# Kernel optimization log

Hardware: AMD Instinct MI355X
Metric: run time of the kernel (lower is better)

Reference implementation:

```python
import jax, jax.numpy as jnp
import numpy as np

B, L, D, H = 2, 2048, 768, 12
HD = D // H  # 64
BASE = 10000


def rope_tables(seq_len, head_dim, base):
    # inverse frequencies over even indices, angles [L, hd/2] -> duplicated to [L, hd]
    inv_freq = 1.0 / (base ** (jnp.arange(0, head_dim, 2, dtype=jnp.float32) / head_dim))
    angles = jnp.arange(seq_len, dtype=jnp.float32)[:, None] * inv_freq[None, :]
    cos = jnp.concatenate([jnp.cos(angles), jnp.cos(angles)], axis=-1)  # [L, hd]
    sin = jnp.concatenate([jnp.sin(angles), jnp.sin(angles)], axis=-1)
    return cos, sin


def rotate_half(x):
    x1, x2 = jnp.split(x, 2, axis=-1)
    return jnp.concatenate([-x2, x1], axis=-1)


def setup_inputs() -> dict:
    key = jax.random.key(0)
    k0, k1, k2 = jax.random.split(key, 3)
    s = 0.02
    return {
        "input_embeddings": jax.random.normal(k0, (B, L, D), dtype=jnp.float32),
        "w_qkv": jax.random.normal(k1, (D, 3 * D), dtype=jnp.float32) * s,
        "b_qkv": jnp.zeros((3 * D,), dtype=jnp.float32),
        "w_out": jax.random.normal(k2, (D, D), dtype=jnp.float32) * s,
        "b_out": jnp.zeros((D,), dtype=jnp.float32),
    }


def reference(input_embeddings, w_qkv, b_qkv, w_out, b_out):
    # QKV projection and head split: b l (h d) -> b h l d
    qkv = input_embeddings @ w_qkv + b_qkv
    q, k, v = jnp.split(qkv, 3, axis=-1)
    to_heads = lambda t: t.reshape(B, L, H, HD).transpose(0, 2, 1, 3)
    q, k, v = map(to_heads, (q, k, v))

    # RoPE (start_pos=0, no kv cache)
    cos, sin = rope_tables(L, HD, BASE)  # [L, HD], broadcasts over b,h
    q = q * cos + rotate_half(q) * sin
    k = k * cos + rotate_half(k) * sin

    # NOTE: source divides by sqrt(d.size(3)) = sqrt(key_seq_len), not sqrt(head_dim)
    scores = jnp.einsum("bhqd,bhkd->bhqk", q, k) / jnp.sqrt(jnp.float32(L))

    causal_mask = jnp.triu(jnp.ones((L, L), dtype=bool), 1)
    neg_inf = -jnp.finfo(scores.dtype).max
    scores = jnp.where(causal_mask, neg_inf, scores)

    probs = jax.nn.softmax(scores, axis=-1)  # dropout disabled (eval)
    attn_out = jnp.einsum("bhqk,bhkd->bhqd", probs, v)
    attn_out = attn_out.transpose(0, 2, 1, 3).reshape(B, L, D)  # b h l d -> b l (h d)
    output = attn_out @ w_out + b_out
    return output, probs
```

## Files before the change

kernel.cpp:

```cpp
#include <hip/hip_runtime.h>
#include <math.h>

#define B_  2
#define L_  2048
#define D_  768
#define H_  12
#define HD_ 64
#define M_  (B_*L_)
#define N3_ (3*D_)
#define OUT_ELEMS ((size_t)B_*L_*D_)

static constexpr float kScale = 0.022097086912079608f;
static constexpr float kLog2_10000_div32 = 0.415241011860920f;

typedef __attribute__((ext_vector_type(8))) short short8;
typedef __attribute__((ext_vector_type(4))) float f32x4;

__device__ __forceinline__ unsigned short f2bf(float f) {
  union { float f; unsigned u; } v; v.f = f;
  unsigned r = v.u + 0x7FFFu + ((v.u >> 16) & 1u);
  return (unsigned short)(r >> 16);
}

__device__ __forceinline__ void async_cp16(const void* g, void* l) {
  __builtin_amdgcn_global_load_lds((const __attribute__((address_space(1))) void*)g,
                                   (__attribute__((address_space(3))) void*)l, 16, 0, 0);
}

__global__ __launch_bounds__(256) void bf16conv_kernel(const float* __restrict__ in,
                                                       unsigned short* __restrict__ out)
{
  const int idx = blockIdx.x * 256 + threadIdx.x;
  const float* src = in + (size_t)idx * 8;
  float4 a = *(const float4*)src;
  float4 b = *(const float4*)(src + 4);
  unsigned short t[8];
  t[0] = f2bf(a.x); t[1] = f2bf(a.y); t[2] = f2bf(a.z); t[3] = f2bf(a.w);
  t[4] = f2bf(b.x); t[5] = f2bf(b.y); t[6] = f2bf(b.z); t[7] = f2bf(b.w);
  *(uint4*)(out + (size_t)idx * 8) = *(uint4*)t;
}

__global__ __launch_bounds__(256) void wtrans_kernel(const float* __restrict__ in,
                                                     unsigned short* __restrict__ out,
                                                     int K, int N)
{
  __shared__ __align__(16) unsigned short T[64][72];
  const int n0 = blockIdx.x * 64;
  const int k0 = blockIdx.y * 64;
  const int tid = threadIdx.x;
  const int row = tid >> 2;
  const int col = (tid & 3) * 16;
  {
    const float* src = in + (size_t)(k0 + row) * N + n0 + col;
    unsigned short tmp[16];
#pragma unroll
    for (int j = 0; j < 16; j += 4) {
      float4 v = *(const float4*)(src + j);
      tmp[j] = f2bf(v.x); tmp[j + 1] = f2bf(v.y); tmp[j + 2] = f2bf(v.z); tmp[j + 3] = f2bf(v.w);
    }
    *(uint4*)&T[row][col]     = *(uint4*)tmp;
    *(uint4*)&T[row][col + 8] = *(uint4*)(tmp + 8);
  }
  __syncthreads();
  unsigned short tmp[16];
#pragma unroll
  for (int j = 0; j < 16; ++j) tmp[j] = T[col + j][row];
  unsigned short* dst = out + (size_t)(n0 + row) * K + k0 + col;
  *(uint4*)dst       = *(uint4*)tmp;
  *(uint4*)(dst + 8) = *(uint4*)(tmp + 8);
}

__global__ __launch_bounds__(256) void vtrans_kernel(const unsigned short* __restrict__ vb,
                                                     unsigned short* __restrict__ vt)
{
  __shared__ __align__(16) unsigned short T[64][72];
  const int bh = blockIdx.y;
  const int l0 = blockIdx.x * 64;
  const int tid = threadIdx.x;
  const int row = tid >> 2;
  const int col = (tid & 3) * 16;
  {
    const unsigned short* src = vb + ((size_t)bh * L_ + l0 + row) * HD_ + col;
    *(uint4*)&T[row][col]     = *(const uint4*)src;
    *(uint4*)&T[row][col + 8] = *(const uint4*)(src + 8);
  }
  __syncthreads();
  unsigned short tmp[16];
#pragma unroll
  for (int j = 0; j < 16; ++j) tmp[j] = T[col + j][row];
  unsigned short* dst = vt + ((size_t)bh * HD_ + row) * L_ + l0 + col;
  *(uint4*)dst       = *(uint4*)tmp;
  *(uint4*)(dst + 8) = *(uint4*)(tmp + 8);
}

__global__ __launch_bounds__(256) void gemm_mfma_kernel(
    const unsigned short* __restrict__ A, const unsigned short* __restrict__ Bt,
    const float* __restrict__ bias, float* __restrict__ C,
    int M, int N, int K, int mode,
    unsigned short* __restrict__ qp, unsigned short* __restrict__ kp,
    unsigned short* __restrict__ vp)
{
  __shared__ __align__(16) unsigned short As[2][128 * 32];
  __shared__ __align__(16) unsigned short Bs[2][128 * 32];

  const int tid  = threadIdx.x;
  const int w    = tid >> 6;
  const int lane = tid & 63;
  const int m16  = lane & 15;
  const int quad = lane >> 4;
  const int wr   = w & 1;
  const int wc   = w >> 1;

  const int bm = blockIdx.y * 128;
  const int bn = blockIdx.x * 128;

  const int s0 = w * 128 + lane;
  const int s1 = s0 + 64;
  const int r0 = s0 >> 2, c0 = (s0 & 3) ^ (r0 & 3);
  const int r1 = s1 >> 2, c1 = (s1 & 3) ^ (r1 & 3);
  const unsigned short* gA0 = A + (size_t)(bm + r0) * K + c0 * 8;
  const unsigned short* gA1 = A + (size_t)(bm + r1) * K + c1 * 8;
  const unsigned short* gB0 = Bt + (size_t)(bn + r0) * K + c0 * 8;
  const unsigned short* gB1 = Bt + (size_t)(bn + r1) * K + c1 * 8;
  const int oS0 = (w * 128) * 8;
  const int oS1 = (w * 128 + 64) * 8;

  const int sw = quad ^ (m16 & 3);
  int offA[4], offB[4];
#pragma unroll
  for (int i = 0; i < 4; ++i) {
    const int ra = wr * 64 + i * 16 + m16;
    const int rb = wc * 64 + i * 16 + m16;
    offA[i] = ra * 32 + sw * 8;
    offB[i] = rb * 32 + sw * 8;
  }

  f32x4 acc[4][4];
#pragma unroll
  for (int i = 0; i < 4; ++i)
#pragma unroll
    for (int j = 0; j < 4; ++j) { acc[i][j][0] = 0.f; acc[i][j][1] = 0.f; acc[i][j][2] = 0.f; acc[i][j][3] = 0.f; }

  async_cp16(gA0, &As[0][oS0]);
  async_cp16(gA1, &As[0][oS1]);
  async_cp16(gB0, &Bs[0][oS0]);
  async_cp16(gB1, &Bs[0][oS1]);
  __syncthreads();

  int cur = 0;
  for (int k0 = 0; k0 < K; k0 += 32) {
    const int nk = k0 + 32;
    if (nk < K) {
      unsigned short* an = &As[cur ^ 1][0];
      unsigned short* bn2 = &Bs[cur ^ 1][0];
      async_cp16(gA0 + nk, an + oS0);
      async_cp16(gA1 + nk, an + oS1);
      async_cp16(gB0 + nk, bn2 + oS0);
      async_cp16(gB1 + nk, bn2 + oS1);
    }
    const unsigned short* Ac = &As[cur][0];
    const unsigned short* Bc = &Bs[cur][0];
    short8 af[4], bfr[4];
#pragma unroll
    for (int i = 0; i < 4; ++i) {
      af[i]  = *(const short8*)(Ac + offA[i]);
      bfr[i] = *(const short8*)(Bc + offB[i]);
    }
#pragma unroll
    for (int i = 0; i < 4; ++i)
#pragma unroll
      for (int j = 0; j < 4; ++j)
        acc[i][j] = __builtin_amdgcn_mfma_f32_16x16x32_bf16(af[i], bfr[j], acc[i][j], 0, 0, 0);
    __syncthreads();
    cur ^= 1;
  }

  if (mode == 0) {
#pragma unroll
    for (int j = 0; j < 4; ++j) {
      const int n = bn + wc * 64 + j * 16 + m16;
      const float bj = bias[n];
#pragma unroll
      for (int i = 0; i < 4; ++i) {
        const int mrow = bm + wr * 64 + i * 16 + quad * 4;
#pragma unroll
        for (int r2 = 0; r2 < 4; ++r2)
          C[(size_t)(mrow + r2) * N + n] = acc[i][j][r2] + bj;
      }
    }
  } else {
    const int segbase = bn + wc * 64;
    const int which = segbase / D_;
    const int h = (segbase - which * D_) >> 6;
    unsigned short* dstT = (which == 0) ? qp : (which == 1) ? kp : vp;
    float bj[4];
#pragma unroll
    for (int og = 0; og < 4; ++og) bj[og] = bias[segbase + og * 16 + m16];
    const float invfA = exp2f(-(float)m16 * kLog2_10000_div32);
    const float invfB = exp2f(-(float)(16 + m16) * kLog2_10000_div32);

#pragma unroll
    for (int i = 0; i < 4; ++i) {
      const int mrow = bm + wr * 64 + i * 16 + quad * 4;
#pragma unroll
      for (int r2 = 0; r2 < 4; ++r2) {
        const int m = mrow + r2;
        const int bi = m >> 11;
        const int li = m & (L_ - 1);
        float vals[4];
#pragma unroll
        for (int og = 0; og < 4; ++og) vals[og] = acc[i][og][r2] + bj[og];
        unsigned short* drow = dstT + (((size_t)(bi * H_ + h)) * L_ + li) * HD_;
        if (which == 2) {
#pragma unroll
          for (int og = 0; og < 4; ++og) drow[og * 16 + m16] = f2bf(vals[og]);
        } else {
          const float fl = (float)li;
#pragma unroll
          for (int og = 0; og < 4; ++og) {
            const int d = og * 16 + m16;
            const float theta = fl * ((og & 1) ? invfB : invfA);
            float sv, cv;
            __sincosf(theta, &sv, &cv);
            const float part = vals[og ^ 2];
            const float rot = (og < 2) ? -part : part;
            drow[d] = f2bf(vals[og] * cv + rot * sv);
          }
        }
      }
    }
  }
}

__global__ __launch_bounds__(256) void attn_mfma_kernel(
    const unsigned short* __restrict__ qb, const unsigned short* __restrict__ kb,
    const unsigned short* __restrict__ vt, float* __restrict__ probs,
    unsigned short* __restrict__ attnb)
{
  __shared__ __align__(16) unsigned short Vs[2][64 * 64];
  __shared__ __align__(16) unsigned short Pb[4][16][72];

  const int tid  = threadIdx.x;
  const int w    = tid >> 6;
  const int lane = tid & 63;
  const int m16  = lane & 15;
  const int quad = lane >> 4;

  const int bh = blockIdx.y;
  const int qt = (int)gridDim.x - 1 - (int)blockIdx.x;
  const int q0 = qt * 64;
  const int bb = bh / H_;
  const int hh = bh - bb * H_;
  const int ktiles = qt + 1;
  const int qrow_base = q0 + w * 16;

  const unsigned short* kbase = kb + (size_t)bh * L_ * HD_;
  const unsigned short* vbase = vt + (size_t)bh * HD_ * L_;

  const unsigned short* qp = qb + ((size_t)bh * L_ + qrow_base + m16) * HD_ + quad * 8;
  const short8 qf0 = *(const short8*)(qp);
  const short8 qf1 = *(const short8*)(qp + 32);

  const unsigned short* kfp = kbase + (size_t)m16 * HD_ + quad * 8;

  float lsum[4] = {0.f, 0.f, 0.f, 0.f};
  for (int kt = 0; kt < ktiles; ++kt) {
    const int k0 = kt * 64;
    short8 kb0[4], kb1[4];
#pragma unroll
    for (int cg = 0; cg < 4; ++cg) {
      const unsigned short* kr = kfp + (size_t)(k0 + cg * 16) * HD_;
      kb0[cg] = *(const short8*)(kr);
      kb1[cg] = *(const short8*)(kr + 32);
    }
#pragma unroll
    for (int cg = 0; cg < 4; ++cg) {
      f32x4 s = {0.f, 0.f, 0.f, 0.f};
      s = __builtin_amdgcn_mfma_f32_16x16x32_bf16(qf0, kb0[cg], s, 0, 0, 0);
      s = __builtin_amdgcn_mfma_f32_16x16x32_bf16(qf1, kb1[cg], s, 0, 0, 0);
      const int kcol = k0 + cg * 16 + m16;
#pragma unroll
      for (int r2 = 0; r2 < 4; ++r2) {
        const int qrow = qrow_base + quad * 4 + r2;
        const float e = __expf(s[r2] * kScale);
        lsum[r2] += (kcol <= qrow) ? e : 0.f;
      }
    }
  }
  float linv[4];
#pragma unroll
  for (int r2 = 0; r2 < 4; ++r2) {
    float v = lsum[r2];
    v += __shfl_xor(v, 1, 64);
    v += __shfl_xor(v, 2, 64);
    v += __shfl_xor(v, 4, 64);
    v += __shfl_xor(v, 8, 64);
    linv[r2] = 1.f / v;
  }

  f32x4 oacc[4];
#pragma unroll
  for (int og = 0; og < 4; ++og) { oacc[og][0]=0.f; oacc[og][1]=0.f; oacc[og][2]=0.f; oacc[og][3]=0.f; }

  const int vs0 = w * 64 + lane;
  const int vs1 = vs0 + 256;
  const int vr0 = vs0 >> 3, vc0 = ((vs0 & 7) ^ (vr0 & 7)) * 8;
  const int vr1 = vs1 >> 3, vc1 = ((vs1 & 7) ^ (vr1 & 7)) * 8;
  const unsigned short* gV0 = vbase + (size_t)vr0 * L_ + vc0;
  const unsigned short* gV1 = vbase + (size_t)vr1 * L_ + vc1;
  const int oV0 = (w * 64) * 8;
  const int oV1 = 2048 + (w * 64) * 8;
  const int swv = m16 & 7;

  async_cp16(gV0, &Vs[0][oV0]);
  async_cp16(gV1, &Vs[0][oV1]);
  __syncthreads();

  int cur = 0;
  for (int kt = 0; kt < ktiles; ++kt) {
    const int k0 = kt * 64;
    if (kt + 1 < ktiles) {
      unsigned short* nb = &Vs[cur ^ 1][0];
      async_cp16(gV0 + k0 + 64, nb + oV0);
      async_cp16(gV1 + k0 + 64, nb + oV1);
    }
    short8 kb0[4], kb1[4];
#pragma unroll
    for (int cg = 0; cg < 4; ++cg) {
      const unsigned short* kr = kfp + (size_t)(k0 + cg * 16) * HD_;
      kb0[cg] = *(const short8*)(kr);
      kb1[cg] = *(const short8*)(kr + 32);
    }
#pragma unroll
    for (int cg = 0; cg < 4; ++cg) {
      f32x4 s = {0.f, 0.f, 0.f, 0.f};
      s = __builtin_amdgcn_mfma_f32_16x16x32_bf16(qf0, kb0[cg], s, 0, 0, 0);
      s = __builtin_amdgcn_mfma_f32_16x16x32_bf16(qf1, kb1[cg], s, 0, 0, 0);
      const int kcol = k0 + cg * 16 + m16;
#pragma unroll
      for (int r2 = 0; r2 < 4; ++r2) {
        const int qrow = qrow_base + quad * 4 + r2;
        const float p = (kcol <= qrow) ? __expf(s[r2] * kScale) * linv[r2] : 0.f;
        probs[((size_t)bh * L_ + qrow) * L_ + kcol] = p;
        Pb[w][quad * 4 + r2][cg * 16 + m16] = f2bf(p);
      }
    }
    const short8 pa0 = *(const short8*)&Pb[w][m16][quad * 8];
    const short8 pa1 = *(const short8*)&Pb[w][m16][32 + quad * 8];
    const unsigned short* Vb = &Vs[cur][0];
#pragma unroll
    for (int og = 0; og < 4; ++og) {
      const int r = og * 16 + m16;
      const short8 v0 = *(const short8*)(Vb + r * 64 + ((quad ^ swv) * 8));
      const short8 v1 = *(const short8*)(Vb + r * 64 + (((quad + 4) ^ swv) * 8));
      oacc[og] = __builtin_amdgcn_mfma_f32_16x16x32_bf16(pa0, v0, oacc[og], 0, 0, 0);
      oacc[og] = __builtin_amdgcn_mfma_f32_16x16x32_bf16(pa1, v1, oacc[og], 0, 0, 0);
    }
    __syncthreads();
    cur ^= 1;
  }

#pragma unroll
  for (int og = 0; og < 4; ++og)
#pragma unroll
    for (int r2 = 0; r2 < 4; ++r2)
      attnb[((size_t)bb * L_ + qrow_base + quad * 4 + r2) * D_ + hh * HD_ + og * 16 + m16] =
          f2bf(oacc[og][r2]);

  {
    const f32x4 z4 = {0.f, 0.f, 0.f, 0.f};
#pragma unroll
    for (int r2 = 0; r2 < 4; ++r2) {
      float* pr = probs + ((size_t)bh * L_ + qrow_base + quad * 4 + r2) * L_;
      for (int c0z = ktiles * 64; c0z < L_; c0z += 64)
        *(f32x4*)(pr + c0z + m16 * 4) = z4;
    }
  }
}

extern "C" void kernel_launch(void* const* d_in, const int* in_sizes, int n_in,
                              void* d_out, int out_size, void* d_ws, size_t ws_size,
                              hipStream_t stream)
{
  const float* x     = (const float*)d_in[0];
  const float* w_qkv = (const float*)d_in[1];
  const float* b_qkv = (const float*)d_in[2];
  const float* w_out = (const float*)d_in[3];
  const float* b_out = (const float*)d_in[4];

  float* out   = (float*)d_out;
  float* probs = out + OUT_ELEMS;

  const size_t NE = (size_t)B_ * H_ * L_ * HD_;
  unsigned short* qbw   = (unsigned short*)d_ws;
  unsigned short* kbw   = qbw + NE;
  unsigned short* vbw   = kbw + NE;
  unsigned short* vtw   = vbw + NE;
  unsigned short* xbw   = vtw + NE;
  unsigned short* attnb = xbw + NE;
  unsigned short* wqT   = attnb + NE;
  unsigned short* woT   = wqT + (size_t)N3_ * D_;

  bf16conv_kernel<<<(int)(OUT_ELEMS / 8 / 256), 256, 0, stream>>>(x, xbw);
  wtrans_kernel<<<dim3(N3_ / 64, D_ / 64), 256, 0, stream>>>(w_qkv, wqT, D_, N3_);
  wtrans_kernel<<<dim3(D_ / 64, D_ / 64), 256, 0, stream>>>(w_out, woT, D_, D_);

  gemm_mfma_kernel<<<dim3(N3_ / 128, M_ / 128), 256, 0, stream>>>(
      xbw, wqT, b_qkv, nullptr, M_, N3_, D_, 1, qbw, kbw, vbw);

  vtrans_kernel<<<dim3(L_ / 64, B_ * H_), 256, 0, stream>>>(vbw, vtw);

  attn_mfma_kernel<<<dim3(L_ / 64, B_ * H_), 256, 0, stream>>>(qbw, kbw, vtw, probs, attnb);

  gemm_mfma_kernel<<<dim3(D_ / 128, M_ / 128), 256, 0, stream>>>(
      attnb, woT, b_out, out, M_, D_, D_, 0, nullptr, nullptr, nullptr);
}
```

Measured before the change: 620.9 us.

## Stage K tiles in shared memory with async double-buffering in both attention passes

K tiles are now loaded cooperatively into swizzled, double-buffered LDS with async copies in both the row-sum pass and the output pass. Previously each wave read K directly from global memory, so the four waves of a block fetched the same K data redundantly. The second pass also raises wave priority around the PV MFMA block. This adds 16 KB of LDS and an extra barrier per tile in the first pass, which may reduce occupancy.

```diff
diff --git a/kernel.cpp b/kernel.cpp
--- a/kernel.cpp
+++ b/kernel.cpp
@@ -237,6 +237,7 @@
     const unsigned short* __restrict__ vt, float* __restrict__ probs,
     unsigned short* __restrict__ attnb)
 {
+  __shared__ __align__(16) unsigned short Ks[2][64 * 64];
   __shared__ __align__(16) unsigned short Vs[2][64 * 64];
   __shared__ __align__(16) unsigned short Pb[4][16][72];
 
@@ -261,30 +262,49 @@
   const short8 qf0 = *(const short8*)(qp);
   const short8 qf1 = *(const short8*)(qp + 32);
 
-  const unsigned short* kfp = kbase + (size_t)m16 * HD_ + quad * 8;
+  const int s0g = tid, s1g = tid + 256;
+  const int r0 = s0g >> 3, c0 = (s0g & 7) ^ (r0 & 7);
+  const int r1 = s1g >> 3, c1 = (s1g & 7) ^ (r1 & 7);
+  const unsigned short* gK0 = kbase + (size_t)r0 * HD_ + c0 * 8;
+  const unsigned short* gK1 = kbase + (size_t)r1 * HD_ + c1 * 8;
+  const unsigned short* gV0 = vbase + (size_t)r0 * L_ + c0 * 8;
+  const unsigned short* gV1 = vbase + (size_t)r1 * L_ + c1 * 8;
+  const int oL0 = (w * 64) * 8;
+  const int oL1 = (256 + w * 64) * 8;
+  const int swk = m16 & 7;
 
   float lsum[4] = {0.f, 0.f, 0.f, 0.f};
-  for (int kt = 0; kt < ktiles; ++kt) {
-    const int k0 = kt * 64;
-    short8 kb0[4], kb1[4];
-#pragma unroll
-    for (int cg = 0; cg < 4; ++cg) {
-      const unsigned short* kr = kfp + (size_t)(k0 + cg * 16) * HD_;
-      kb0[cg] = *(const short8*)(kr);
-      kb1[cg] = *(const short8*)(kr + 32);
-    }
-#pragma unroll
-    for (int cg = 0; cg < 4; ++cg) {
-      f32x4 s = {0.f, 0.f, 0.f, 0.f};
-      s = __builtin_amdgcn_mfma_f32_16x16x32_bf16(qf0, kb0[cg], s, 0, 0, 0);
-      s = __builtin_amdgcn_mfma_f32_16x16x32_bf16(qf1, kb1[cg], s, 0, 0, 0);
-      const int kcol = k0 + cg * 16 + m16;
-#pragma unroll
-      for (int r2 = 0; r2 < 4; ++r2) {
-        const int qrow = qrow_base + quad * 4 + r2;
-        const float e = __expf(s[r2] * kScale);
-        lsum[r2] += (kcol <= qrow) ? e : 0.f;
-      }
+  {
+    async_cp16(gK0, &Ks[0][oL0]);
+    async_cp16(gK1, &Ks[0][oL1]);
+    __syncthreads();
+    int cur = 0;
+    for (int kt = 0; kt < ktiles; ++kt) {
+      const int k0 = kt * 64;
+      if (kt + 1 < ktiles) {
+        const size_t adv = (size_t)(kt + 1) * 64 * HD_;
+        async_cp16(gK0 + adv, &Ks[cur ^ 1][oL0]);
+        async_cp16(gK1 + adv, &Ks[cur ^ 1][oL1]);
+      }
+      const unsigned short* Kc = &Ks[cur][0];
+#pragma unroll
+      for (int cg = 0; cg < 4; ++cg) {
+        const int r = cg * 16 + m16;
+        const short8 b0 = *(const short8*)(Kc + r * 64 + ((quad ^ swk) * 8));
+        const short8 b1 = *(const short8*)(Kc + r * 64 + (((quad + 4) ^ swk) * 8));
+        f32x4 s = {0.f, 0.f, 0.f, 0.f};
+        s = __builtin_amdgcn_mfma_f32_16x16x32_bf16(qf0, b0, s, 0, 0, 0);
+        s = __builtin_amdgcn_mfma_f32_16x16x32_bf16(qf1, b1, s, 0, 0, 0);
+        const int kcol = k0 + cg * 16 + m16;
+#pragma unroll
+        for (int r2 = 0; r2 < 4; ++r2) {
+          const int qrow = qrow_base + quad * 4 + r2;
+          const float e = __expf(s[r2] * kScale);
+          lsum[r2] += (kcol <= qrow) ? e : 0.f;
+        }
+      }
+      __syncthreads();
+      cur ^= 1;
     }
   }
   float linv[4];
@@ -302,62 +322,57 @@
 #pragma unroll
   for (int og = 0; og < 4; ++og) { oacc[og][0]=0.f; oacc[og][1]=0.f; oacc[og][2]=0.f; oacc[og][3]=0.f; }
 
-  const int vs0 = w * 64 + lane;
-  const int vs1 = vs0 + 256;
-  const int vr0 = vs0 >> 3, vc0 = ((vs0 & 7) ^ (vr0 & 7)) * 8;
-  const int vr1 = vs1 >> 3, vc1 = ((vs1 & 7) ^ (vr1 & 7)) * 8;
-  const unsigned short* gV0 = vbase + (size_t)vr0 * L_ + vc0;
-  const unsigned short* gV1 = vbase + (size_t)vr1 * L_ + vc1;
-  const int oV0 = (w * 64) * 8;
-  const int oV1 = 2048 + (w * 64) * 8;
-  const int swv = m16 & 7;
-
-  async_cp16(gV0, &Vs[0][oV0]);
-  async_cp16(gV1, &Vs[0][oV1]);
-  __syncthreads();
-
-  int cur = 0;
-  for (int kt = 0; kt < ktiles; ++kt) {
-    const int k0 = kt * 64;
-    if (kt + 1 < ktiles) {
-      unsigned short* nb = &Vs[cur ^ 1][0];
-      async_cp16(gV0 + k0 + 64, nb + oV0);
-      async_cp16(gV1 + k0 + 64, nb + oV1);
-    }
-    short8 kb0[4], kb1[4];
-#pragma unroll
-    for (int cg = 0; cg < 4; ++cg) {
-      const unsigned short* kr = kfp + (size_t)(k0 + cg * 16) * HD_;
-      kb0[cg] = *(const short8*)(kr);
-      kb1[cg] = *(const short8*)(kr + 32);
-    }
-#pragma unroll
-    for (int cg = 0; cg < 4; ++cg) {
-      f32x4 s = {0.f, 0.f, 0.f, 0.f};
-      s = __builtin_amdgcn_mfma_f32_16x16x32_bf16(qf0, kb0[cg], s, 0, 0, 0);
-      s = __builtin_amdgcn_mfma_f32_16x16x32_bf16(qf1, kb1[cg], s, 0, 0, 0);
-      const int kcol = k0 + cg * 16 + m16;
-#pragma unroll
-      for (int r2 = 0; r2 < 4; ++r2) {
-        const int qrow = qrow_base + quad * 4 + r2;
-        const float p = (kcol <= qrow) ? __expf(s[r2] * kScale) * linv[r2] : 0.f;
-        probs[((size_t)bh * L_ + qrow) * L_ + kcol] = p;
-        Pb[w][quad * 4 + r2][cg * 16 + m16] = f2bf(p);
-      }
-    }
-    const short8 pa0 = *(const short8*)&Pb[w][m16][quad * 8];
-    const short8 pa1 = *(const short8*)&Pb[w][m16][32 + quad * 8];
-    const unsigned short* Vb = &Vs[cur][0];
-#pragma unroll
-    for (int og = 0; og < 4; ++og) {
-      const int r = og * 16 + m16;
-      const short8 v0 = *(const short8*)(Vb + r * 64 + ((quad ^ swv) * 8));
-      const short8 v1 = *(const short8*)(Vb + r * 64 + (((quad + 4) ^ swv) * 8));
-      oacc[og] = __builtin_amdgcn_mfma_f32_16x16x32_bf16(pa0, v0, oacc[og], 0, 0, 0);
-      oacc[og] = __builtin_amdgcn_mfma_f32_16x16x32_bf16(pa1, v1, oacc[og], 0, 0, 0);
-    }
+  {
+    async_cp16(gK0, &Ks[0][oL0]);
+    async_cp16(gK1, &Ks[0][oL1]);
+    async_cp16(gV0, &Vs[0][oL0]);
+    async_cp16(gV1, &Vs[0][oL1]);
     __syncthreads();
-    cur ^= 1;
+    int cur = 0;
+    for (int kt = 0; kt < ktiles; ++kt) {
+      const int k0 = kt * 64;
+      if (kt + 1 < ktiles) {
+        const size_t advK = (size_t)(kt + 1) * 64 * HD_;
+        const int advV = (kt + 1) * 64;
+        async_cp16(gK0 + advK, &Ks[cur ^ 1][oL0]);
+        async_cp16(gK1 + advK, &Ks[cur ^ 1][oL1]);
+        async_cp16(gV0 + advV, &Vs[cur ^ 1][oL0]);
+        async_cp16(gV1 + advV, &Vs[cur ^ 1][oL1]);
+      }
+      const unsigned short* Kc = &Ks[cur][0];
+      const unsigned short* Vc = &Vs[cur][0];
+#pragma unroll
+      for (int cg = 0; cg < 4; ++cg) {
+        const int r = cg * 16 + m16;
+        const short8 b0 = *(const short8*)(Kc + r * 64 + ((quad ^ swk) * 8));
+        const short8 b1 = *(const short8*)(Kc + r * 64 + (((quad + 4) ^ swk) * 8));
+        f32x4 s = {0.f, 0.f, 0.f, 0.f};
+        s = __builtin_amdgcn_mfma_f32_16x16x32_bf16(qf0, b0, s, 0, 0, 0);
+        s = __builtin_amdgcn_mfma_f32_16x16x32_bf16(qf1, b1, s, 0, 0, 0);
+        const int kcol = k0 + cg * 16 + m16;
+#pragma unroll
+        for (int r2 = 0; r2 < 4; ++r2) {
+          const int qrow = qrow_base + quad * 4 + r2;
+          const float p = (kcol <= qrow) ? __expf(s[r2] * kScale) * linv[r2] : 0.f;
+          probs[((size_t)bh * L_ + qrow) * L_ + kcol] = p;
+          Pb[w][quad * 4 + r2][cg * 16 + m16] = f2bf(p);
+        }
+      }
+      const short8 pa0 = *(const short8*)&Pb[w][m16][quad * 8];
+      const short8 pa1 = *(const short8*)&Pb[w][m16][32 + quad * 8];
+      __builtin_amdgcn_s_setprio(1);
+#pragma unroll
+      for (int og = 0; og < 4; ++og) {
+        const int r = og * 16 + m16;
+        const short8 v0 = *(const short8*)(Vc + r * 64 + ((quad ^ swk) * 8));
+        const short8 v1 = *(const short8*)(Vc + r * 64 + (((quad + 4) ^ swk) * 8));
+        oacc[og] = __builtin_amdgcn_mfma_f32_16x16x32_bf16(pa0, v0, oacc[og], 0, 0, 0);
+        oacc[og] = __builtin_amdgcn_mfma_f32_16x16x32_bf16(pa1, v1, oacc[og], 0, 0, 0);
+      }
+      __builtin_amdgcn_s_setprio(0);
+      __syncthreads();
+      cur ^= 1;
+    }
   }
 
 #pragma unroll
```

Result: faster. 542.1 us (-12.7%).
